# Kernel optimization log

Measured on AMD Instinct MI355X. Metric: run time of the kernel, lower is better.

The kernel has to match this reference:

```python
import jax, jax.numpy as jnp
import numpy as np

INPUT_DIM = 1024
HEADS = 16
HEAD_DIM = 64
OUT_DIM = HEADS * HEAD_DIM
B, S = 4, 2048


def _xavier(key, shape):
    fan_in, fan_out = shape
    limit = float(np.sqrt(6.0 / (fan_in + fan_out)))
    return jax.random.uniform(key, shape, jnp.float32, -limit, limit)


def setup_inputs() -> dict:
    key = jax.random.key(0)
    kq, kk, kv, kwq, kwk, kwv = jax.random.split(key, 6)
    return {
        "query": jax.random.normal(kq, (B, S, INPUT_DIM), jnp.float32),
        "key": jax.random.normal(kk, (B, S, INPUT_DIM), jnp.float32),
        "value": jax.random.normal(kv, (B, S, INPUT_DIM), jnp.float32),
        "WQ": _xavier(kwq, (INPUT_DIM, OUT_DIM)),
        "WK": _xavier(kwk, (INPUT_DIM, OUT_DIM)),
        "WV": _xavier(kwv, (INPUT_DIM, OUT_DIM)),
    }


def reference(query, key, value, WQ, WK, WV):
    b, s, _ = query.shape
    # Project and split into heads: [B, H, S, D]
    q = (query @ WQ).reshape(b, s, HEADS, HEAD_DIM).transpose(0, 2, 1, 3)
    k = (key @ WK).reshape(b, s, HEADS, HEAD_DIM).transpose(0, 2, 1, 3)
    v = (value @ WV).reshape(b, s, HEADS, HEAD_DIM).transpose(0, 2, 1, 3)
    scores = jnp.einsum("bhqd,bhkd->bhqk", q, k) / jnp.sqrt(
        jnp.asarray(HEAD_DIM, q.dtype)
    )
    attn = jax.nn.softmax(scores, axis=-1)
    out = jnp.einsum("bhqk,bhkd->bhqd", attn, v)
    return out.transpose(0, 2, 1, 3).reshape(b, s, OUT_DIM)
```

## Files before the change

kernel.cpp:

```cpp
#include <hip/hip_runtime.h>
#include <stdint.h>

#define HEADS 16
#define HDIM  64
#define NDIM  1024
#define BATCH 4
#define SEQ   2048
#define MTOT  (BATCH * SEQ)

typedef __attribute__((ext_vector_type(8))) short short8;
typedef __attribute__((ext_vector_type(4))) float float4v;
typedef __attribute__((ext_vector_type(4))) int int4v;
typedef __attribute__((ext_vector_type(4))) unsigned short ushort4v;

static __device__ __forceinline__ unsigned int fbits(float f) {
    union { float f; unsigned int u; } v; v.f = f; return v.u;
}
static __device__ __forceinline__ unsigned short bf16r(float f) {
    return (unsigned short)((fbits(f) + 0x8000u) >> 16);
}
static __device__ __forceinline__ unsigned int pack2(float lo, float hi) {
    return ((fbits(hi) + 0x8000u) & 0xffff0000u) | ((fbits(lo) + 0x8000u) >> 16);
}

static __device__ __forceinline__ void gl_lds16(const unsigned short* g, unsigned short* l) {
    __builtin_amdgcn_global_load_lds(
        (const __attribute__((address_space(1))) unsigned int*)(uintptr_t)g,
        (__attribute__((address_space(3))) unsigned int*)(uintptr_t)l,
        16, 0, 0);
}

__global__ __launch_bounds__(256) void cast_x(
    const float* __restrict__ X0, const float* __restrict__ X1, const float* __restrict__ X2,
    unsigned short* __restrict__ Y0, unsigned short* __restrict__ Y1, unsigned short* __restrict__ Y2)
{
    int z = blockIdx.z;
    const float* X = (z == 0) ? X0 : (z == 1) ? X1 : X2;
    unsigned short* Y = (z == 0) ? Y0 : (z == 1) ? Y1 : Y2;
    size_t i = ((size_t)blockIdx.x * 256 + threadIdx.x) * 8;
    float4v a = *(const float4v*)(X + i);
    float4v b = *(const float4v*)(X + i + 4);
    int4v p;
    p.x = pack2(a.x, a.y); p.y = pack2(a.z, a.w);
    p.z = pack2(b.x, b.y); p.w = pack2(b.z, b.w);
    *(int4v*)(Y + i) = p;
}

__global__ __launch_bounds__(256) void cast_transpose_w(
    const float* __restrict__ W0, const float* __restrict__ W1, const float* __restrict__ W2,
    unsigned short* __restrict__ T0, unsigned short* __restrict__ T1, unsigned short* __restrict__ T2)
{
    const float* W = (blockIdx.z == 0) ? W0 : (blockIdx.z == 1) ? W1 : W2;
    unsigned short* T = (blockIdx.z == 0) ? T0 : (blockIdx.z == 1) ? T1 : T2;
    __shared__ __align__(16) unsigned short tile[64][65];
    int t = threadIdx.x;
    int k0 = blockIdx.y * 64, n0 = blockIdx.x * 64;
    int row = t >> 2, seg = (t & 3) * 16;
    const float* src = W + (size_t)(k0 + row) * NDIM + n0 + seg;
#pragma unroll
    for (int i = 0; i < 4; ++i) {
        float4v v = *(const float4v*)(src + i * 4);
        tile[row][seg + i*4 + 0] = bf16r(v.x);
        tile[row][seg + i*4 + 1] = bf16r(v.y);
        tile[row][seg + i*4 + 2] = bf16r(v.z);
        tile[row][seg + i*4 + 3] = bf16r(v.w);
    }
    __syncthreads();
    unsigned short* dst = T + (size_t)(n0 + row) * NDIM + k0 + seg;
#pragma unroll
    for (int i = 0; i < 4; ++i) {
        ushort4v o;
        o.x = tile[seg + i*4 + 0][row];
        o.y = tile[seg + i*4 + 1][row];
        o.z = tile[seg + i*4 + 2][row];
        o.w = tile[seg + i*4 + 3][row];
        *(ushort4v*)(dst + i*4) = o;
    }
}

#define BM 128
#define BN 128
#define BK 32

__global__ __launch_bounds__(256) void proj_gemm(
    const unsigned short* __restrict__ Xqc, const unsigned short* __restrict__ Xkc,
    const unsigned short* __restrict__ Xvc, const float* __restrict__ Xv32,
    const unsigned short* __restrict__ Tq, const unsigned short* __restrict__ Tk, const unsigned short* __restrict__ Tv,
    unsigned short* __restrict__ Oq, unsigned short* __restrict__ Ok, unsigned short* __restrict__ Ov,
    float qscale, int vasync)
{
    int z = blockIdx.z;
    const unsigned short* Xc = (z == 0) ? Xqc : (z == 1) ? Xkc : Xvc;
    const unsigned short* Wt = (z == 0) ? Tq : (z == 1) ? Tk : Tv;
    unsigned short* Out = (z == 0) ? Oq : (z == 1) ? Ok : Ov;
    float scale = (z == 0) ? qscale : 1.0f;
    bool vtrans = (z == 2);
    bool afast = (z < 2) || (vasync != 0);

    __shared__ __align__(16) unsigned short Asm[BM * BK];
    __shared__ __align__(16) unsigned short Bsm[BN * BK];

    int t = threadIdx.x;
    int wave = t >> 6, lane = t & 63, l15 = lane & 15, quad = lane >> 4;
    int m0 = blockIdx.x * BM, n0 = blockIdx.y * BN;
    int wm = (wave >> 1) * 64, wn = (wave & 1) * 64;

    float4v acc[4][4];
#pragma unroll
    for (int i = 0; i < 4; ++i)
#pragma unroll
        for (int j = 0; j < 4; ++j) acc[i][j] = (float4v){0.f, 0.f, 0.f, 0.f};

    int c0 = t, c1 = t + 256;
    const unsigned short* ga0 = Xc + (size_t)(m0 + (c0 >> 2)) * NDIM + (c0 & 3) * 8;
    const unsigned short* ga1 = Xc + (size_t)(m0 + (c1 >> 2)) * NDIM + (c1 & 3) * 8;
    const float* fa0 = Xv32 + (size_t)(m0 + (c0 >> 2)) * NDIM + (c0 & 3) * 8;
    const float* fa1 = Xv32 + (size_t)(m0 + (c1 >> 2)) * NDIM + (c1 & 3) * 8;
    const unsigned short* gb0 = Wt + (size_t)(n0 + (c0 >> 2)) * NDIM + (c0 & 3) * 8;
    const unsigned short* gb1 = Wt + (size_t)(n0 + (c1 >> 2)) * NDIM + (c1 & 3) * 8;
    unsigned short* as0 = &Asm[c0 * 8];
    unsigned short* as1 = &Asm[c1 * 8];
    unsigned short* bs0 = &Bsm[c0 * 8];
    unsigned short* bs1 = &Bsm[c1 * 8];

    for (int kt = 0; kt < NDIM; kt += BK) {
        __syncthreads();
        if (afast) {
            gl_lds16(ga0 + kt, as0);
            gl_lds16(ga1 + kt, as1);
        } else {
            float4v x0 = *(const float4v*)(fa0 + kt);
            float4v x1 = *(const float4v*)(fa0 + kt + 4);
            float4v y0 = *(const float4v*)(fa1 + kt);
            float4v y1 = *(const float4v*)(fa1 + kt + 4);
            int4v pa0, pa1;
            pa0.x = pack2(x0.x, x0.y); pa0.y = pack2(x0.z, x0.w);
            pa0.z = pack2(x1.x, x1.y); pa0.w = pack2(x1.z, x1.w);
            pa1.x = pack2(y0.x, y0.y); pa1.y = pack2(y0.z, y0.w);
            pa1.z = pack2(y1.x, y1.y); pa1.w = pack2(y1.z, y1.w);
            *(int4v*)as0 = pa0;
            *(int4v*)as1 = pa1;
        }
        gl_lds16(gb0 + kt, bs0);
        gl_lds16(gb1 + kt, bs1);
        __syncthreads();

        short8 af[4], bfr[4];
#pragma unroll
        for (int mt = 0; mt < 4; ++mt)
            af[mt] = *(const short8*)&Asm[(wm + mt * 16 + l15) * BK + quad * 8];
#pragma unroll
        for (int nt = 0; nt < 4; ++nt)
            bfr[nt] = *(const short8*)&Bsm[(wn + nt * 16 + l15) * BK + quad * 8];
#pragma unroll
        for (int mt = 0; mt < 4; ++mt)
#pragma unroll
            for (int nt = 0; nt < 4; ++nt)
                acc[mt][nt] = __builtin_amdgcn_mfma_f32_16x16x32_bf16(af[mt], bfr[nt], acc[mt][nt], 0, 0, 0);
    }

#pragma unroll
    for (int mt = 0; mt < 4; ++mt) {
        int mbase = m0 + wm + mt * 16 + quad * 4;
        int b = mbase >> 11;
        int s = mbase & 2047;
#pragma unroll
        for (int nt = 0; nt < 4; ++nt) {
            int gn = n0 + wn + nt * 16 + l15;
            int h = gn >> 6, d = gn & 63;
            if (!vtrans) {
                size_t base = ((size_t)((b * HEADS + h) * SEQ + s)) * HDIM + d;
#pragma unroll
                for (int r = 0; r < 4; ++r)
                    Out[base + (size_t)r * HDIM] = bf16r(acc[mt][nt][r] * scale);
            } else {
                size_t base = ((size_t)((b * HEADS + h) * HDIM + d)) * SEQ + s;
                ushort4v o;
                o.x = bf16r(acc[mt][nt][0]);
                o.y = bf16r(acc[mt][nt][1]);
                o.z = bf16r(acc[mt][nt][2]);
                o.w = bf16r(acc[mt][nt][3]);
                *(ushort4v*)(Out + base) = o;
            }
        }
    }
}

#define BQ  128
#define BKC 64

__global__ __launch_bounds__(256) void attn_kernel(
    const unsigned short* __restrict__ Q,
    const unsigned short* __restrict__ K,
    const unsigned short* __restrict__ Vt,
    float* __restrict__ Out)
{
    __shared__ __align__(16) unsigned short Ksm[BKC][72];
    __shared__ __align__(16) unsigned short Vsm[HDIM][72];
    __shared__ __align__(16) unsigned short Psm[4][32][72];

    int t = threadIdx.x;
    int wave = t >> 6, lane = t & 63, l15 = lane & 15, quad = lane >> 4;
    int L = blockIdx.x;
    int bh = L & 63;
    int b = bh >> 4, h = bh & 15;
    int q0 = (L >> 6) * BQ;

    const unsigned short* Qbh = Q + (size_t)bh * SEQ * HDIM;
    const unsigned short* Kbh = K + (size_t)bh * SEQ * HDIM;
    const unsigned short* Vbh = Vt + (size_t)bh * HDIM * SEQ;

    short8 qf[2][2];
#pragma unroll
    for (int mt = 0; mt < 2; ++mt) {
        int qr = q0 + wave * 32 + mt * 16 + l15;
        qf[mt][0] = *(const short8*)(Qbh + (size_t)qr * HDIM + quad * 8);
        qf[mt][1] = *(const short8*)(Qbh + (size_t)qr * HDIM + 32 + quad * 8);
    }

    float lsum[2][4];
    float4v acc_o[2][4];
#pragma unroll
    for (int mt = 0; mt < 2; ++mt) {
#pragma unroll
        for (int r = 0; r < 4; ++r) lsum[mt][r] = 0.f;
#pragma unroll
        for (int dtt = 0; dtt < 4; ++dtt) acc_o[mt][dtt] = (float4v){0.f, 0.f, 0.f, 0.f};
    }

    int srow = t >> 2;
    int sseg = (t & 3) * 16;
    const unsigned short* kptr = Kbh + (size_t)srow * HDIM + sseg;
    const unsigned short* vptr = Vbh + (size_t)srow * SEQ + sseg;

    short8 kv0 = *(const short8*)(kptr);
    short8 kv1 = *(const short8*)(kptr + 8);
    short8 kv2 = *(const short8*)(vptr);
    short8 kv3 = *(const short8*)(vptr + 8);

    for (int kc = 0; kc < SEQ; kc += BKC) {
        __syncthreads();
        *(short8*)&Ksm[srow][sseg]     = kv0;
        *(short8*)&Ksm[srow][sseg + 8] = kv1;
        *(short8*)&Vsm[srow][sseg]     = kv2;
        *(short8*)&Vsm[srow][sseg + 8] = kv3;
        __syncthreads();

        int kn = kc + BKC;
        if (kn < SEQ) {
            kv0 = *(const short8*)(kptr + (size_t)kn * HDIM);
            kv1 = *(const short8*)(kptr + (size_t)kn * HDIM + 8);
            kv2 = *(const short8*)(vptr + kn);
            kv3 = *(const short8*)(vptr + kn + 8);
        }

        float4v sc[2][4];
#pragma unroll
        for (int mt = 0; mt < 2; ++mt)
#pragma unroll
            for (int nt = 0; nt < 4; ++nt) sc[mt][nt] = (float4v){0.f, 0.f, 0.f, 0.f};
#pragma unroll
        for (int nt = 0; nt < 4; ++nt) {
            short8 kf0 = *(const short8*)&Ksm[l15 * 4 + nt][quad * 8];
            short8 kf1 = *(const short8*)&Ksm[l15 * 4 + nt][32 + quad * 8];
#pragma unroll
            for (int mt = 0; mt < 2; ++mt) {
                sc[mt][nt] = __builtin_amdgcn_mfma_f32_16x16x32_bf16(qf[mt][0], kf0, sc[mt][nt], 0, 0, 0);
                sc[mt][nt] = __builtin_amdgcn_mfma_f32_16x16x32_bf16(qf[mt][1], kf1, sc[mt][nt], 0, 0, 0);
            }
        }

#pragma unroll
        for (int mt = 0; mt < 2; ++mt)
#pragma unroll
            for (int r = 0; r < 4; ++r) {
                float p0 = __builtin_amdgcn_exp2f(sc[mt][0][r]);
                float p1 = __builtin_amdgcn_exp2f(sc[mt][1][r]);
                float p2 = __builtin_amdgcn_exp2f(sc[mt][2][r]);
                float p3 = __builtin_amdgcn_exp2f(sc[mt][3][r]);
                lsum[mt][r] += (p0 + p1) + (p2 + p3);
                int row = mt * 16 + quad * 4 + r;
                ushort4v pp;
                pp.x = bf16r(p0); pp.y = bf16r(p1);
                pp.z = bf16r(p2); pp.w = bf16r(p3);
                *(ushort4v*)&Psm[wave][row][l15 * 4] = pp;
            }

#pragma unroll
        for (int kseg = 0; kseg < 2; ++kseg) {
            short8 pf0 = *(const short8*)&Psm[wave][l15][kseg * 32 + quad * 8];
            short8 pf1 = *(const short8*)&Psm[wave][16 + l15][kseg * 32 + quad * 8];
#pragma unroll
            for (int dtt = 0; dtt < 4; ++dtt) {
                short8 vf = *(const short8*)&Vsm[dtt * 16 + l15][kseg * 32 + quad * 8];
                acc_o[0][dtt] = __builtin_amdgcn_mfma_f32_16x16x32_bf16(pf0, vf, acc_o[0][dtt], 0, 0, 0);
                acc_o[1][dtt] = __builtin_amdgcn_mfma_f32_16x16x32_bf16(pf1, vf, acc_o[1][dtt], 0, 0, 0);
            }
        }
    }

#pragma unroll
    for (int mt = 0; mt < 2; ++mt)
#pragma unroll
        for (int r = 0; r < 4; ++r) {
            float l = lsum[mt][r];
            l += __shfl_xor(l, 1);
            l += __shfl_xor(l, 2);
            l += __shfl_xor(l, 4);
            l += __shfl_xor(l, 8);
            float inv = 1.0f / l;
            int qrow = q0 + wave * 32 + mt * 16 + quad * 4 + r;
            size_t base = ((size_t)(b * SEQ + qrow)) * NDIM + h * HDIM;
#pragma unroll
            for (int dtt = 0; dtt < 4; ++dtt)
                Out[base + dtt * 16 + l15] = acc_o[mt][dtt][r] * inv;
        }
}

extern "C" void kernel_launch(void* const* d_in, const int* in_sizes, int n_in,
                              void* d_out, int out_size, void* d_ws, size_t ws_size,
                              hipStream_t stream)
{
    const float* q_in = (const float*)d_in[0];
    const float* k_in = (const float*)d_in[1];
    const float* v_in = (const float*)d_in[2];
    const float* WQ = (const float*)d_in[3];
    const float* WK = (const float*)d_in[4];
    const float* WV = (const float*)d_in[5];
    float* out = (float*)d_out;

    unsigned short* ws = (unsigned short*)d_ws;
    size_t wsz = (size_t)NDIM * NDIM;
    size_t psz = (size_t)MTOT * NDIM;
    unsigned short* Tq = ws;
    unsigned short* Tk = Tq + wsz;
    unsigned short* Tv = Tk + wsz;
    unsigned short* Qp = Tv + wsz;
    unsigned short* Kp = Qp + psz;
    unsigned short* Vp = Kp + psz;
    unsigned short* Xvc = Vp + psz;

    unsigned short* Xqc = (unsigned short*)d_out;
    unsigned short* Xkc = Xqc + psz;

    size_t need = (3 * wsz + 4 * psz) * sizeof(unsigned short);
    int vasync = (ws_size >= need) ? 1 : 0;

    cast_x<<<dim3(MTOT * NDIM / (256 * 8), 1, vasync ? 3 : 2), 256, 0, stream>>>(
        q_in, k_in, v_in, Xqc, Xkc, Xvc);
    cast_transpose_w<<<dim3(16, 16, 3), 256, 0, stream>>>(WQ, WK, WV, Tq, Tk, Tv);
    proj_gemm<<<dim3(MTOT / BM, NDIM / BN, 3), 256, 0, stream>>>(
        Xqc, Xkc, Xvc, v_in, Tq, Tk, Tv, Qp, Kp, Vp, 0.125f * 1.44269504088896f, vasync);
    attn_kernel<<<dim3(SEQ / BQ * BATCH * HEADS), 256, 0, stream>>>(Qp, Kp, Vp, out);
}
```

Measured before the change: 310.2 us.

## Restructure attention to 32x32 MFMA with register-resident P and no LDS staging

The attention kernel now uses 32x32x16 bf16 MFMAs and computes the transposed score tile with K as the A operand. The exponentiated probabilities then land in registers already in the layout the PV MFMA needs, which removes the LDS round trip for P. K and V are loaded straight from global memory per wave instead of being staged through shared memory, so the per-chunk __syncthreads are gone. Each wave now owns 64 query rows, giving 256 per block, with a launch bound of 2 blocks per CU. The trade-off is that each wave re-reads K and V from cache on its own, and register pressure rises.

New measurement: 395.4 us. 27.5% more time.

```diff
diff --git a/kernel.cpp b/kernel.cpp
--- a/kernel.cpp
+++ b/kernel.cpp
@@ -9,7 +9,9 @@
 #define MTOT  (BATCH * SEQ)
 
 typedef __attribute__((ext_vector_type(8))) short short8;
+typedef __attribute__((ext_vector_type(4))) short short4s;
 typedef __attribute__((ext_vector_type(4))) float float4v;
+typedef __attribute__((ext_vector_type(16))) float float16v;
 typedef __attribute__((ext_vector_type(4))) int int4v;
 typedef __attribute__((ext_vector_type(4))) unsigned short ushort4v;
 
@@ -186,135 +188,145 @@
     }
 }
 
-#define BQ  128
+#define BQW 64
+#define BQ  (BQW * 4)
 #define BKC 64
 
-__global__ __launch_bounds__(256) void attn_kernel(
+__global__ __launch_bounds__(256, 2) void attn_kernel(
     const unsigned short* __restrict__ Q,
     const unsigned short* __restrict__ K,
     const unsigned short* __restrict__ Vt,
     float* __restrict__ Out)
 {
-    __shared__ __align__(16) unsigned short Ksm[BKC][72];
-    __shared__ __align__(16) unsigned short Vsm[HDIM][72];
-    __shared__ __align__(16) unsigned short Psm[4][32][72];
+    __shared__ float lbuf[4][64];
 
     int t = threadIdx.x;
-    int wave = t >> 6, lane = t & 63, l15 = lane & 15, quad = lane >> 4;
+    int wave = t >> 6, lane = t & 63;
+    int l31 = lane & 31, h = lane >> 5;
     int L = blockIdx.x;
     int bh = L & 63;
-    int b = bh >> 4, h = bh & 15;
-    int q0 = (L >> 6) * BQ;
+    int b = bh >> 4, hh = bh & 15;
+    int q0 = (L >> 6) * BQ + wave * BQW;
 
     const unsigned short* Qbh = Q + (size_t)bh * SEQ * HDIM;
     const unsigned short* Kbh = K + (size_t)bh * SEQ * HDIM;
     const unsigned short* Vbh = Vt + (size_t)bh * HDIM * SEQ;
 
-    short8 qf[2][2];
-#pragma unroll
-    for (int mt = 0; mt < 2; ++mt) {
-        int qr = q0 + wave * 32 + mt * 16 + l15;
-        qf[mt][0] = *(const short8*)(Qbh + (size_t)qr * HDIM + quad * 8);
-        qf[mt][1] = *(const short8*)(Qbh + (size_t)qr * HDIM + 32 + quad * 8);
-    }
-
-    float lsum[2][4];
-    float4v acc_o[2][4];
-#pragma unroll
-    for (int mt = 0; mt < 2; ++mt) {
-#pragma unroll
-        for (int r = 0; r < 4; ++r) lsum[mt][r] = 0.f;
-#pragma unroll
-        for (int dtt = 0; dtt < 4; ++dtt) acc_o[mt][dtt] = (float4v){0.f, 0.f, 0.f, 0.f};
-    }
-
-    int srow = t >> 2;
-    int sseg = (t & 3) * 16;
-    const unsigned short* kptr = Kbh + (size_t)srow * HDIM + sseg;
-    const unsigned short* vptr = Vbh + (size_t)srow * SEQ + sseg;
-
-    short8 kv0 = *(const short8*)(kptr);
-    short8 kv1 = *(const short8*)(kptr + 8);
-    short8 kv2 = *(const short8*)(vptr);
-    short8 kv3 = *(const short8*)(vptr + 8);
+    short8 qf[2][4];
+#pragma unroll
+    for (int mt = 0; mt < 2; ++mt)
+#pragma unroll
+        for (int kk = 0; kk < 4; ++kk)
+            qf[mt][kk] = *(const short8*)(Qbh + (size_t)(q0 + mt * 32 + l31) * HDIM + kk * 16 + h * 8);
+
+    float16v Oa[2][2];
+#pragma unroll
+    for (int mt = 0; mt < 2; ++mt)
+#pragma unroll
+        for (int dt = 0; dt < 2; ++dt)
+#pragma unroll
+            for (int r = 0; r < 16; ++r) Oa[mt][dt][r] = 0.f;
+    float lsum[2] = {0.f, 0.f};
+
+    short8 kf[2][4];
+#pragma unroll
+    for (int kt = 0; kt < 2; ++kt)
+#pragma unroll
+        for (int kk = 0; kk < 4; ++kk)
+            kf[kt][kk] = *(const short8*)(Kbh + (size_t)(kt * 32 + l31) * HDIM + kk * 16 + h * 8);
 
     for (int kc = 0; kc < SEQ; kc += BKC) {
-        __syncthreads();
-        *(short8*)&Ksm[srow][sseg]     = kv0;
-        *(short8*)&Ksm[srow][sseg + 8] = kv1;
-        *(short8*)&Vsm[srow][sseg]     = kv2;
-        *(short8*)&Vsm[srow][sseg + 8] = kv3;
-        __syncthreads();
+        short4s vld[2][2][4];
+#pragma unroll
+        for (int dt = 0; dt < 2; ++dt)
+#pragma unroll
+            for (int kt = 0; kt < 2; ++kt) {
+                const unsigned short* vb = Vbh + (size_t)(dt * 32 + l31) * SEQ + kc + kt * 32 + h * 4;
+#pragma unroll
+                for (int i = 0; i < 4; ++i)
+                    vld[dt][kt][i] = *(const short4s*)(vb + i * 8);
+            }
+
+        float16v S[2][2];
+#pragma unroll
+        for (int kt = 0; kt < 2; ++kt)
+#pragma unroll
+            for (int mt = 0; mt < 2; ++mt) {
+#pragma unroll
+                for (int r = 0; r < 16; ++r) S[kt][mt][r] = 0.f;
+#pragma unroll
+                for (int kk = 0; kk < 4; ++kk)
+                    S[kt][mt] = __builtin_amdgcn_mfma_f32_32x32x16_bf16(kf[kt][kk], qf[mt][kk], S[kt][mt], 0, 0, 0);
+            }
 
         int kn = kc + BKC;
         if (kn < SEQ) {
-            kv0 = *(const short8*)(kptr + (size_t)kn * HDIM);
-            kv1 = *(const short8*)(kptr + (size_t)kn * HDIM + 8);
-            kv2 = *(const short8*)(vptr + kn);
-            kv3 = *(const short8*)(vptr + kn + 8);
+#pragma unroll
+            for (int kt = 0; kt < 2; ++kt)
+#pragma unroll
+                for (int kk = 0; kk < 4; ++kk)
+                    kf[kt][kk] = *(const short8*)(Kbh + (size_t)(kn + kt * 32 + l31) * HDIM + kk * 16 + h * 8);
         }
 
-        float4v sc[2][4];
-#pragma unroll
-        for (int mt = 0; mt < 2; ++mt)
-#pragma unroll
-            for (int nt = 0; nt < 4; ++nt) sc[mt][nt] = (float4v){0.f, 0.f, 0.f, 0.f};
-#pragma unroll
-        for (int nt = 0; nt < 4; ++nt) {
-            short8 kf0 = *(const short8*)&Ksm[l15 * 4 + nt][quad * 8];
-            short8 kf1 = *(const short8*)&Ksm[l15 * 4 + nt][32 + quad * 8];
+        short8 pf[2][2][2];
+#pragma unroll
+        for (int kt = 0; kt < 2; ++kt)
 #pragma unroll
             for (int mt = 0; mt < 2; ++mt) {
-                sc[mt][nt] = __builtin_amdgcn_mfma_f32_16x16x32_bf16(qf[mt][0], kf0, sc[mt][nt], 0, 0, 0);
-                sc[mt][nt] = __builtin_amdgcn_mfma_f32_16x16x32_bf16(qf[mt][1], kf1, sc[mt][nt], 0, 0, 0);
+                float p[16];
+                float s8 = 0.f;
+#pragma unroll
+                for (int r = 0; r < 16; ++r) {
+                    p[r] = __builtin_amdgcn_exp2f(S[kt][mt][r]);
+                    s8 += p[r];
+                }
+                lsum[mt] += s8;
+#pragma unroll
+                for (int s = 0; s < 2; ++s) {
+                    int4v pk;
+                    pk.x = pack2(p[s*8+0], p[s*8+1]);
+                    pk.y = pack2(p[s*8+2], p[s*8+3]);
+                    pk.z = pack2(p[s*8+4], p[s*8+5]);
+                    pk.w = pack2(p[s*8+6], p[s*8+7]);
+                    union { int4v i; short8 s; } cv; cv.i = pk;
+                    pf[kt][mt][s] = cv.s;
+                }
             }
+
+#pragma unroll
+        for (int kt = 0; kt < 2; ++kt)
+#pragma unroll
+            for (int s = 0; s < 2; ++s)
+#pragma unroll
+                for (int dt = 0; dt < 2; ++dt) {
+                    short8 vbf = __builtin_shufflevector(vld[dt][kt][2*s], vld[dt][kt][2*s+1],
+                                                         0, 1, 2, 3, 4, 5, 6, 7);
+#pragma unroll
+                    for (int mt = 0; mt < 2; ++mt)
+                        Oa[mt][dt] = __builtin_amdgcn_mfma_f32_32x32x16_bf16(pf[kt][mt][s], vbf, Oa[mt][dt], 0, 0, 0);
+                }
+    }
+
+#pragma unroll
+    for (int mt = 0; mt < 2; ++mt) {
+        float l = lsum[mt] + __shfl_xor(lsum[mt], 32);
+        if (lane < 32) lbuf[wave][mt * 32 + l31] = l;
+    }
+    __syncthreads();
+
+#pragma unroll
+    for (int mt = 0; mt < 2; ++mt) {
+#pragma unroll
+        for (int r = 0; r < 16; ++r) {
+            int qoff = (r & 3) + 8 * (r >> 2) + 4 * h;
+            float inv = 1.0f / lbuf[wave][mt * 32 + qoff];
+            int qrow = q0 + mt * 32 + qoff;
+            size_t base = ((size_t)(b * SEQ + qrow)) * NDIM + hh * HDIM;
+#pragma unroll
+            for (int dt = 0; dt < 2; ++dt)
+                Out[base + dt * 32 + l31] = Oa[mt][dt][r] * inv;
         }
-
-#pragma unroll
-        for (int mt = 0; mt < 2; ++mt)
-#pragma unroll
-            for (int r = 0; r < 4; ++r) {
-                float p0 = __builtin_amdgcn_exp2f(sc[mt][0][r]);
-                float p1 = __builtin_amdgcn_exp2f(sc[mt][1][r]);
-                float p2 = __builtin_amdgcn_exp2f(sc[mt][2][r]);
-                float p3 = __builtin_amdgcn_exp2f(sc[mt][3][r]);
-                lsum[mt][r] += (p0 + p1) + (p2 + p3);
-                int row = mt * 16 + quad * 4 + r;
-                ushort4v pp;
-                pp.x = bf16r(p0); pp.y = bf16r(p1);
-                pp.z = bf16r(p2); pp.w = bf16r(p3);
-                *(ushort4v*)&Psm[wave][row][l15 * 4] = pp;
-            }
-
-#pragma unroll
-        for (int kseg = 0; kseg < 2; ++kseg) {
-            short8 pf0 = *(const short8*)&Psm[wave][l15][kseg * 32 + quad * 8];
-            short8 pf1 = *(const short8*)&Psm[wave][16 + l15][kseg * 32 + quad * 8];
-#pragma unroll
-            for (int dtt = 0; dtt < 4; ++dtt) {
-                short8 vf = *(const short8*)&Vsm[dtt * 16 + l15][kseg * 32 + quad * 8];
-                acc_o[0][dtt] = __builtin_amdgcn_mfma_f32_16x16x32_bf16(pf0, vf, acc_o[0][dtt], 0, 0, 0);
-                acc_o[1][dtt] = __builtin_amdgcn_mfma_f32_16x16x32_bf16(pf1, vf, acc_o[1][dtt], 0, 0, 0);
-            }
-        }
-    }
-
-#pragma unroll
-    for (int mt = 0; mt < 2; ++mt)
-#pragma unroll
-        for (int r = 0; r < 4; ++r) {
-            float l = lsum[mt][r];
-            l += __shfl_xor(l, 1);
-            l += __shfl_xor(l, 2);
-            l += __shfl_xor(l, 4);
-            l += __shfl_xor(l, 8);
-            float inv = 1.0f / l;
-            int qrow = q0 + wave * 32 + mt * 16 + quad * 4 + r;
-            size_t base = ((size_t)(b * SEQ + qrow)) * NDIM + h * HDIM;
-#pragma unroll
-            for (int dtt = 0; dtt < 4; ++dtt)
-                Out[base + dtt * 16 + l15] = acc_o[mt][dtt][r] * inv;
-        }
+    }
 }
 
 extern "C" void kernel_launch(void* const* d_in, const int* in_sizes, int n_in,
```
